# Performance work log

Measured on AMD Instinct MI355X. Metric: run time of the kernel, lower is better.

Reference implementation:

```python
import jax, jax.numpy as jnp
import numpy as np

M = 16384          # test points
N = 16384          # train points
D = 2              # (kx, ky)
CHUNK = 8192       # rows of K_star per chunk (matches torch default)


def setup_inputs() -> dict:
    key = jax.random.key(0)
    k1, k2, k3 = jax.random.split(key, 3)
    X_test = jax.random.normal(k1, (M, D), dtype=jnp.float32)
    X_train = jax.random.normal(k2, (N, D), dtype=jnp.float32)
    alpha = jax.random.normal(k3, (N, 2), dtype=jnp.float32)  # dual vars [Re, Im]
    log_lengthscale = jnp.asarray(np.log(0.1), dtype=jnp.float32)
    log_outputscale = jnp.asarray(np.log(1.0), dtype=jnp.float32)
    return {
        "X_test": X_test,
        "X_train": X_train,
        "alpha": alpha,
        "log_lengthscale": log_lengthscale,
        "log_outputscale": log_outputscale,
    }


def reference(X_test, X_train, alpha, log_lengthscale, log_outputscale):
    """Posterior mean mu* = K_rbf(X_test, X_train) @ alpha, chunked over test rows."""
    ell2 = jnp.exp(log_lengthscale) ** 2
    sf2 = jnp.exp(log_outputscale) ** 2
    xt_sq = jnp.sum(X_train * X_train, axis=1)  # (N,)

    def chunk_fn(xc):  # xc: (CHUNK, D)
        # squared euclidean distances (clamped at 0 for numerical safety)
        sq = (jnp.sum(xc * xc, axis=1)[:, None]
              + xt_sq[None, :]
              - 2.0 * (xc @ X_train.T))          # (CHUNK, N)
        sq = jnp.maximum(sq, 0.0)
        K = sf2 * jnp.exp(-0.5 * sq / ell2)      # RBF kernel values
        return K @ alpha                          # (CHUNK, 2)

    m = X_test.shape[0]
    chunks = X_test.reshape(m // CHUNK, CHUNK, D)
    out = jax.lax.map(chunk_fn, chunks)           # (m//CHUNK, CHUNK, 2)
    return out.reshape(m, 2)
```

## Files before the change

### kernel.cpp

```cpp
#include <hip/hip_runtime.h>
#include <math.h>

#define M_PTS 16384
#define N_PTS 16384
#define TPB 256
#define SPLITS 128
#define CHUNK_N (N_PTS / SPLITS)
#define PTS 4
#define TEST_BLOCKS (M_PTS / (TPB * PTS))

__device__ __forceinline__ float fexp2(float x) {
#if __has_builtin(__builtin_amdgcn_exp2f)
    return __builtin_amdgcn_exp2f(x);
#else
    return exp2f(x);
#endif
}

__device__ __forceinline__ void gatomic_fadd(float* p, float v) {
    asm volatile("global_atomic_add_f32 %0, %1, off" :: "v"(p), "v"(v) : "memory");
}

template <bool ATOMIC>
__global__ __launch_bounds__(TPB, 8) void gp_fused(
        const float2* __restrict__ Xte,
        const float2* __restrict__ Xtr,
        const float2* __restrict__ alpha,
        const float* __restrict__ log_ell,
        const float* __restrict__ log_sf,
        float2* __restrict__ outp) {
    __shared__ float4 sSt[CHUNK_N];
    __shared__ float  sA1[CHUNK_N];

    const int tid = threadIdx.x;
    const float ell = expf(log_ell[0]);
    const float c = -0.5f / (ell * ell) * 1.4426950408889634f;

    const int j0 = blockIdx.y * CHUNK_N;
    if (tid < CHUNK_N) {
        const float sf2 = expf(2.0f * log_sf[0]);
        float2 t = Xtr[j0 + tid];
        float2 a = alpha[j0 + tid];
        sSt[tid] = make_float4(-2.0f * c * t.x, -2.0f * c * t.y,
                               c * (t.x * t.x + t.y * t.y), sf2 * a.x);
        sA1[tid] = sf2 * a.y;
    }

    const int base = blockIdx.x * (TPB * PTS) + tid;
    float2 x0 = Xte[base];
    float2 x1 = Xte[base + TPB];
    float2 x2 = Xte[base + 2 * TPB];
    float2 x3 = Xte[base + 3 * TPB];
    const float b0 = c * (x0.x * x0.x + x0.y * x0.y);
    const float b1 = c * (x1.x * x1.x + x1.y * x1.y);
    const float b2 = c * (x2.x * x2.x + x2.y * x2.y);
    const float b3 = c * (x3.x * x3.x + x3.y * x3.y);

    __syncthreads();

    float a00 = 0.f, a01 = 0.f, a10 = 0.f, a11 = 0.f;
    float a20 = 0.f, a21 = 0.f, a30 = 0.f, a31 = 0.f;

#pragma unroll 2
    for (int j = 0; j < CHUNK_N; ++j) {
        float4 s = sSt[j];
        float w1 = sA1[j];
        float t0 = fminf(fmaf(s.x, x0.x, fmaf(s.y, x0.y, b0 + s.z)), 0.0f);
        float t1 = fminf(fmaf(s.x, x1.x, fmaf(s.y, x1.y, b1 + s.z)), 0.0f);
        float t2 = fminf(fmaf(s.x, x2.x, fmaf(s.y, x2.y, b2 + s.z)), 0.0f);
        float t3 = fminf(fmaf(s.x, x3.x, fmaf(s.y, x3.y, b3 + s.z)), 0.0f);
        float e0 = fexp2(t0);
        float e1 = fexp2(t1);
        float e2 = fexp2(t2);
        float e3 = fexp2(t3);
        a00 = fmaf(e0, s.w, a00); a01 = fmaf(e0, w1, a01);
        a10 = fmaf(e1, s.w, a10); a11 = fmaf(e1, w1, a11);
        a20 = fmaf(e2, s.w, a20); a21 = fmaf(e2, w1, a21);
        a30 = fmaf(e3, s.w, a30); a31 = fmaf(e3, w1, a31);
    }

    if (ATOMIC) {
        float* o = (float*)outp;
        gatomic_fadd(&o[2 * base], a00);            gatomic_fadd(&o[2 * base + 1], a01);
        gatomic_fadd(&o[2 * (base + TPB)], a10);     gatomic_fadd(&o[2 * (base + TPB) + 1], a11);
        gatomic_fadd(&o[2 * (base + 2 * TPB)], a20); gatomic_fadd(&o[2 * (base + 2 * TPB) + 1], a21);
        gatomic_fadd(&o[2 * (base + 3 * TPB)], a30); gatomic_fadd(&o[2 * (base + 3 * TPB) + 1], a31);
    } else {
        float2* w = outp + (size_t)blockIdx.y * M_PTS;
        w[base]           = make_float2(a00, a01);
        w[base + TPB]     = make_float2(a10, a11);
        w[base + 2 * TPB] = make_float2(a20, a21);
        w[base + 3 * TPB] = make_float2(a30, a31);
    }
}

__global__ __launch_bounds__(TPB) void reduce_kernel(
        const float2* __restrict__ ws, float2* __restrict__ out) {
    int i = blockIdx.x * blockDim.x + threadIdx.x;
    float sx = 0.f, sy = 0.f;
#pragma unroll 8
    for (int k = 0; k < SPLITS; ++k) {
        float2 v = ws[(size_t)k * M_PTS + i];
        sx += v.x;
        sy += v.y;
    }
    out[i] = make_float2(sx, sy);
}

extern "C" void kernel_launch(void* const* d_in, const int* in_sizes, int n_in,
                              void* d_out, int out_size, void* d_ws, size_t ws_size,
                              hipStream_t stream) {
    const float2* Xte = (const float2*)d_in[0];
    const float2* Xtr = (const float2*)d_in[1];
    const float2* alpha = (const float2*)d_in[2];
    const float* log_ell = (const float*)d_in[3];
    const float* log_sf = (const float*)d_in[4];

    dim3 grid(TEST_BLOCKS, SPLITS);
    const size_t need = (size_t)SPLITS * M_PTS * sizeof(float2);

    if (ws_size >= need) {
        float2* partials = (float2*)d_ws;
        gp_fused<false><<<grid, TPB, 0, stream>>>(Xte, Xtr, alpha, log_ell, log_sf,
                                                  partials);
        reduce_kernel<<<M_PTS / TPB, TPB, 0, stream>>>(partials, (float2*)d_out);
    } else {
        hipMemsetAsync(d_out, 0, (size_t)out_size * sizeof(float), stream);
        gp_fused<true><<<grid, TPB, 0, stream>>>(Xte, Xtr, alpha, log_ell, log_sf,
                                                 (float2*)d_out);
    }
}
```

Measured before the change: 122.5 us.

## Bin points on a spatial grid and evaluate RBF only over neighbouring cells

Replaces the all-pairs dense RBF accumulation with a uniform 2D cell grid. Training and test points are binned by histogram, prefix-scan and scatter kernels, and test points are padded to whole wavefronts per cell. Each wavefront then visits only the 5x5 neighbouring training cells and skips exp work when the whole wave is below a cutoff exponent. This cuts the number of kernel evaluations but adds several small preprocessing launches, uncoalesced global loads in place of shared-memory reuse, and truncation of tiny kernel values. A full-range fallback runs when the lengthscale is too large for the cell size.

Result: slower. 207.1 us (+69.1%).

```diff
diff --git a/kernel.cpp b/kernel.cpp
--- a/kernel.cpp
+++ b/kernel.cpp
@@ -4,10 +4,30 @@
 #define M_PTS 16384
 #define N_PTS 16384
 #define TPB 256
-#define SPLITS 128
-#define CHUNK_N (N_PTS / SPLITS)
-#define PTS 4
-#define TEST_BLOCKS (M_PTS / (TPB * PTS))
+
+#define NC 28
+#define NCELLS (NC * NC)
+#define H 0.375f
+#define INV_H (1.0f / 0.375f)
+#define ORIG (-5.25f)
+#define TCUT 40.0f
+
+#define NPAD_MAX (M_PTS + NCELLS * 63)
+#define WAVES_MAX (M_PTS / 64 + NCELLS)
+#define KITEMS 25
+#define ITEMS_MAX (WAVES_MAX * KITEMS)
+#define MAIN_BLOCKS (ITEMS_MAX / 4)
+
+#define OFF_HDR 0
+#define OFF_TRC 256
+#define OFF_TEC (OFF_TRC + NCELLS * 4)
+#define OFF_TRS (OFF_TEC + NCELLS * 4)
+#define OFF_TRCUR (OFF_TRS + NCELLS * 4)
+#define OFF_TECUR (OFF_TRCUR + NCELLS * 4)
+#define OFF_TRA (OFF_TECUR + NCELLS * 4)
+#define OFF_TRW1 (OFF_TRA + N_PTS * 16)
+#define OFF_T4 (OFF_TRW1 + N_PTS * 4)
+#define WS_NEED (OFF_T4 + (size_t)NPAD_MAX * 16)
 
 __device__ __forceinline__ float fexp2(float x) {
 #if __has_builtin(__builtin_amdgcn_exp2f)
@@ -21,90 +41,183 @@
     asm volatile("global_atomic_add_f32 %0, %1, off" :: "v"(p), "v"(v) : "memory");
 }
 
-template <bool ATOMIC>
-__global__ __launch_bounds__(TPB, 8) void gp_fused(
-        const float2* __restrict__ Xte,
-        const float2* __restrict__ Xtr,
-        const float2* __restrict__ alpha,
-        const float* __restrict__ log_ell,
-        const float* __restrict__ log_sf,
-        float2* __restrict__ outp) {
-    __shared__ float4 sSt[CHUNK_N];
-    __shared__ float  sA1[CHUNK_N];
-
+__device__ __forceinline__ int cellco(float v) {
+    int c = (int)floorf((v - ORIG) * INV_H);
+    return min(NC - 1, max(0, c));
+}
+
+
+__global__ void fill_kernel(float4* __restrict__ T4) {
+    int i = blockIdx.x * blockDim.x + threadIdx.x;
+    if (i < NPAD_MAX)
+        T4[i] = make_float4(0.f, 0.f, -3.0e38f, __int_as_float(-1));
+}
+
+__global__ void hist_kernel(const float2* __restrict__ Xtr,
+                            const float2* __restrict__ Xte,
+                            int* __restrict__ trc, int* __restrict__ tec) {
+    int i = blockIdx.x * blockDim.x + threadIdx.x;
+    if (i >= N_PTS) return;
+    float2 t = Xtr[i];
+    atomicAdd(&trc[cellco(t.y) * NC + cellco(t.x)], 1);
+    float2 x = Xte[i];
+    atomicAdd(&tec[cellco(x.y) * NC + cellco(x.x)], 1);
+}
+
+__global__ __launch_bounds__(1024) void scan_kernel(
+        const int* __restrict__ trc, const int* __restrict__ tec,
+        int* __restrict__ trs, int* __restrict__ trcur,
+        int* __restrict__ tecur, int* __restrict__ hdr) {
+    __shared__ int sc[1024];
+    int tid = threadIdx.x;
+    int v = (tid < NCELLS) ? trc[tid] : 0;
+    sc[tid] = v; __syncthreads();
+    for (int off = 1; off < 1024; off <<= 1) {
+        int u = (tid >= off) ? sc[tid - off] : 0;
+        __syncthreads();
+        sc[tid] += u;
+        __syncthreads();
+    }
+    if (tid < NCELLS) { int e = sc[tid] - v; trs[tid] = e; trcur[tid] = e; }
+    __syncthreads();
+    int pv = (tid < NCELLS) ? ((tec[tid] + 63) & ~63) : 0;
+    sc[tid] = pv; __syncthreads();
+    for (int off = 1; off < 1024; off <<= 1) {
+        int u = (tid >= off) ? sc[tid - off] : 0;
+        __syncthreads();
+        sc[tid] += u;
+        __syncthreads();
+    }
+    if (tid < NCELLS) tecur[tid] = sc[tid] - pv;
+    if (tid == NCELLS - 1) hdr[0] = sc[tid] / 64;
+}
+
+__global__ void scatter_kernel(const float2* __restrict__ Xtr,
+                               const float2* __restrict__ Xte,
+                               const float2* __restrict__ alpha,
+                               const float* __restrict__ log_ell,
+                               const float* __restrict__ log_sf,
+                               int* __restrict__ trcur, int* __restrict__ tecur,
+                               float4* __restrict__ trA, float* __restrict__ trW1,
+                               float4* __restrict__ T4) {
+    int i = blockIdx.x * blockDim.x + threadIdx.x;
+    if (i >= N_PTS) return;
+    float ell = expf(log_ell[0]);
+    float sf2 = expf(2.0f * log_sf[0]);
+    float c = -0.5f / (ell * ell) * 1.4426950408889634f;
+
+    float2 t = Xtr[i];
+    float2 a = alpha[i];
+    int ct = cellco(t.y) * NC + cellco(t.x);
+    int pt = atomicAdd(&trcur[ct], 1);
+    trA[pt] = make_float4(-2.f * c * t.x, -2.f * c * t.y,
+                          c * (t.x * t.x + t.y * t.y), sf2 * a.x);
+    trW1[pt] = sf2 * a.y;
+
+    float2 x = Xte[i];
+    int cx = cellco(x.y) * NC + cellco(x.x);
+    int px = atomicAdd(&tecur[cx], 1);
+    T4[px] = make_float4(x.x, x.y, c * (x.x * x.x + x.y * x.y), __int_as_float(i));
+}
+
+__global__ __launch_bounds__(TPB, 8) void gp_sparse(
+        const float4* __restrict__ T4, const float4* __restrict__ trA,
+        const float* __restrict__ trW1, const int* __restrict__ trs,
+        const int* __restrict__ trc, const int* __restrict__ hdr,
+        const float* __restrict__ log_ell, float* __restrict__ out) {
+    const int wave = (blockIdx.x << 2) + (threadIdx.x >> 6);
+    const int lane = threadIdx.x & 63;
+    const int tw = wave / KITEMS;
+    const int k = wave - tw * KITEMS;
+    if (tw >= hdr[0]) return;
+
+    const float ell = expf(log_ell[0]);
+    const float cmag = 0.5f / (ell * ell) * 1.4426950408889634f;
+    const bool fb = (TCUT / cmag) > (4.0f * H * H);
+
+    float4 tp = T4[tw * 64 + lane];
+    const float x = tp.x, y = tp.y, b = tp.z;
+    const int oidx = __float_as_int(tp.w);
+
+    int js, je;
+    if (fb) {
+        if (k != 12) return;
+        js = 0; je = N_PTS;
+    } else {
+        int cx = __builtin_amdgcn_readfirstlane(cellco(x));
+        int cy = __builtin_amdgcn_readfirstlane(cellco(y));
+        int tcx = cx + (k % 5) - 2;
+        int tcy = cy + (k / 5) - 2;
+        if (tcx < 0 || tcx >= NC || tcy < 0 || tcy >= NC) return;
+        int cid = tcy * NC + tcx;
+        js = trs[cid];
+        je = js + trc[cid];
+    }
+
+    float a0 = 0.f, a1 = 0.f;
+#pragma unroll 2
+    for (int j = js; j < je; ++j) {
+        float4 tv = trA[j];
+        float t = fmaf(tv.x, x, fmaf(tv.y, y, b + tv.z));
+        if (__ballot(t > -TCUT) != 0ull) {
+            float e = fexp2(t);
+            a0 = fmaf(e, tv.w, a0);
+            a1 = fmaf(e, trW1[j], a1);
+        }
+    }
+
+    if (oidx >= 0 && ((a0 != 0.f) || (a1 != 0.f))) {
+        gatomic_fadd(&out[2 * oidx], a0);
+        gatomic_fadd(&out[2 * oidx + 1], a1);
+    }
+}
+
+__global__ __launch_bounds__(TPB, 8) void gp_dense(
+        const float2* __restrict__ Xte, const float2* __restrict__ Xtr,
+        const float2* __restrict__ alpha, const float* __restrict__ log_ell,
+        const float* __restrict__ log_sf, float* __restrict__ out) {
+    __shared__ float4 sSt[128];
+    __shared__ float sA1[128];
     const int tid = threadIdx.x;
     const float ell = expf(log_ell[0]);
     const float c = -0.5f / (ell * ell) * 1.4426950408889634f;
-
-    const int j0 = blockIdx.y * CHUNK_N;
-    if (tid < CHUNK_N) {
+    const int j0 = blockIdx.y * 128;
+    if (tid < 128) {
         const float sf2 = expf(2.0f * log_sf[0]);
         float2 t = Xtr[j0 + tid];
         float2 a = alpha[j0 + tid];
-        sSt[tid] = make_float4(-2.0f * c * t.x, -2.0f * c * t.y,
+        sSt[tid] = make_float4(-2.f * c * t.x, -2.f * c * t.y,
                                c * (t.x * t.x + t.y * t.y), sf2 * a.x);
         sA1[tid] = sf2 * a.y;
     }
-
-    const int base = blockIdx.x * (TPB * PTS) + tid;
-    float2 x0 = Xte[base];
-    float2 x1 = Xte[base + TPB];
-    float2 x2 = Xte[base + 2 * TPB];
-    float2 x3 = Xte[base + 3 * TPB];
+    const int base = blockIdx.x * (TPB * 4) + tid;
+    float2 x0 = Xte[base], x1 = Xte[base + TPB];
+    float2 x2 = Xte[base + 2 * TPB], x3 = Xte[base + 3 * TPB];
     const float b0 = c * (x0.x * x0.x + x0.y * x0.y);
     const float b1 = c * (x1.x * x1.x + x1.y * x1.y);
     const float b2 = c * (x2.x * x2.x + x2.y * x2.y);
     const float b3 = c * (x3.x * x3.x + x3.y * x3.y);
-
     __syncthreads();
-
     float a00 = 0.f, a01 = 0.f, a10 = 0.f, a11 = 0.f;
     float a20 = 0.f, a21 = 0.f, a30 = 0.f, a31 = 0.f;
-
 #pragma unroll 2
-    for (int j = 0; j < CHUNK_N; ++j) {
+    for (int j = 0; j < 128; ++j) {
         float4 s = sSt[j];
         float w1 = sA1[j];
-        float t0 = fminf(fmaf(s.x, x0.x, fmaf(s.y, x0.y, b0 + s.z)), 0.0f);
-        float t1 = fminf(fmaf(s.x, x1.x, fmaf(s.y, x1.y, b1 + s.z)), 0.0f);
-        float t2 = fminf(fmaf(s.x, x2.x, fmaf(s.y, x2.y, b2 + s.z)), 0.0f);
-        float t3 = fminf(fmaf(s.x, x3.x, fmaf(s.y, x3.y, b3 + s.z)), 0.0f);
-        float e0 = fexp2(t0);
-        float e1 = fexp2(t1);
-        float e2 = fexp2(t2);
-        float e3 = fexp2(t3);
+        float t0 = fminf(fmaf(s.x, x0.x, fmaf(s.y, x0.y, b0 + s.z)), 0.f);
+        float t1 = fminf(fmaf(s.x, x1.x, fmaf(s.y, x1.y, b1 + s.z)), 0.f);
+        float t2 = fminf(fmaf(s.x, x2.x, fmaf(s.y, x2.y, b2 + s.z)), 0.f);
+        float t3 = fminf(fmaf(s.x, x3.x, fmaf(s.y, x3.y, b3 + s.z)), 0.f);
+        float e0 = fexp2(t0), e1 = fexp2(t1), e2 = fexp2(t2), e3 = fexp2(t3);
         a00 = fmaf(e0, s.w, a00); a01 = fmaf(e0, w1, a01);
         a10 = fmaf(e1, s.w, a10); a11 = fmaf(e1, w1, a11);
         a20 = fmaf(e2, s.w, a20); a21 = fmaf(e2, w1, a21);
         a30 = fmaf(e3, s.w, a30); a31 = fmaf(e3, w1, a31);
     }
-
-    if (ATOMIC) {
-        float* o = (float*)outp;
-        gatomic_fadd(&o[2 * base], a00);            gatomic_fadd(&o[2 * base + 1], a01);
-        gatomic_fadd(&o[2 * (base + TPB)], a10);     gatomic_fadd(&o[2 * (base + TPB) + 1], a11);
-        gatomic_fadd(&o[2 * (base + 2 * TPB)], a20); gatomic_fadd(&o[2 * (base + 2 * TPB) + 1], a21);
-        gatomic_fadd(&o[2 * (base + 3 * TPB)], a30); gatomic_fadd(&o[2 * (base + 3 * TPB) + 1], a31);
-    } else {
-        float2* w = outp + (size_t)blockIdx.y * M_PTS;
-        w[base]           = make_float2(a00, a01);
-        w[base + TPB]     = make_float2(a10, a11);
-        w[base + 2 * TPB] = make_float2(a20, a21);
-        w[base + 3 * TPB] = make_float2(a30, a31);
-    }
-}
-
-__global__ __launch_bounds__(TPB) void reduce_kernel(
-        const float2* __restrict__ ws, float2* __restrict__ out) {
-    int i = blockIdx.x * blockDim.x + threadIdx.x;
-    float sx = 0.f, sy = 0.f;
-#pragma unroll 8
-    for (int k = 0; k < SPLITS; ++k) {
-        float2 v = ws[(size_t)k * M_PTS + i];
-        sx += v.x;
-        sy += v.y;
-    }
-    out[i] = make_float2(sx, sy);
+    gatomic_fadd(&out[2 * base], a00);             gatomic_fadd(&out[2 * base + 1], a01);
+    gatomic_fadd(&out[2 * (base + TPB)], a10);      gatomic_fadd(&out[2 * (base + TPB) + 1], a11);
+    gatomic_fadd(&out[2 * (base + 2 * TPB)], a20);  gatomic_fadd(&out[2 * (base + 2 * TPB) + 1], a21);
+    gatomic_fadd(&out[2 * (base + 3 * TPB)], a30);  gatomic_fadd(&out[2 * (base + 3 * TPB) + 1], a31);
 }
 
 extern "C" void kernel_launch(void* const* d_in, const int* in_sizes, int n_in,
@@ -115,18 +228,33 @@
     const float2* alpha = (const float2*)d_in[2];
     const float* log_ell = (const float*)d_in[3];
     const float* log_sf = (const float*)d_in[4];
-
-    dim3 grid(TEST_BLOCKS, SPLITS);
-    const size_t need = (size_t)SPLITS * M_PTS * sizeof(float2);
-
-    if (ws_size >= need) {
-        float2* partials = (float2*)d_ws;
-        gp_fused<false><<<grid, TPB, 0, stream>>>(Xte, Xtr, alpha, log_ell, log_sf,
-                                                  partials);
-        reduce_kernel<<<M_PTS / TPB, TPB, 0, stream>>>(partials, (float2*)d_out);
+    float* out = (float*)d_out;
+
+    hipMemsetAsync(out, 0, (size_t)out_size * sizeof(float), stream);
+
+    if (ws_size >= WS_NEED) {
+        char* ws = (char*)d_ws;
+        int* hdr = (int*)(ws + OFF_HDR);
+        int* trc = (int*)(ws + OFF_TRC);
+        int* tec = (int*)(ws + OFF_TEC);
+        int* trs = (int*)(ws + OFF_TRS);
+        int* trcur = (int*)(ws + OFF_TRCUR);
+        int* tecur = (int*)(ws + OFF_TECUR);
+        float4* trA = (float4*)(ws + OFF_TRA);
+        float* trW1 = (float*)(ws + OFF_TRW1);
+        float4* T4 = (float4*)(ws + OFF_T4);
+
+        hipMemsetAsync(trc, 0, NCELLS * 2 * sizeof(int), stream);
+        fill_kernel<<<(NPAD_MAX + TPB - 1) / TPB, TPB, 0, stream>>>(T4);
+        hist_kernel<<<N_PTS / TPB, TPB, 0, stream>>>(Xtr, Xte, trc, tec);
+        scan_kernel<<<1, 1024, 0, stream>>>(trc, tec, trs, trcur, tecur, hdr);
+        scatter_kernel<<<N_PTS / TPB, TPB, 0, stream>>>(Xtr, Xte, alpha, log_ell,
+                                                        log_sf, trcur, tecur,
+                                                        trA, trW1, T4);
+        gp_sparse<<<MAIN_BLOCKS, TPB, 0, stream>>>(T4, trA, trW1, trs, trc, hdr,
+                                                   log_ell, out);
     } else {
-        hipMemsetAsync(d_out, 0, (size_t)out_size * sizeof(float), stream);
-        gp_fused<true><<<grid, TPB, 0, stream>>>(Xte, Xtr, alpha, log_ell, log_sf,
-                                                 (float2*)d_out);
-    }
-}
+        dim3 grid(M_PTS / (TPB * 4), N_PTS / 128);
+        gp_dense<<<grid, TPB, 0, stream>>>(Xte, Xtr, alpha, log_ell, log_sf, out);
+    }
+}
```

## Replace dense RBF sum with cell-list neighbor search and exponent cutoff

Applied to the files above, without the earlier changes.

Training points are binned into a uniform 2D grid by a histogram, a prefix scan and a scatter, which also precompute the per-point kernel coefficients. A per-test-point wavefront then evaluates only the grid rows and columns inside a cutoff radius where the base-2 exponent stays above -20, instead of all N training points. If the lengthscale makes the radius too large, it falls back to scanning every training point. The aim is to avoid most of the exp and FMA work of the dense O(M·N) evaluation, at the cost of a truncation error, several extra small launches, and gather-style global loads in place of shared-memory reuse.

Result: faster. 118.8 us (-3.0%).

```diff
diff --git a/kernel.cpp b/kernel.cpp
--- a/kernel.cpp
+++ b/kernel.cpp
@@ -3,11 +3,22 @@
 
 #define M_PTS 16384
 #define N_PTS 16384
-#define TPB 256
-#define SPLITS 128
-#define CHUNK_N (N_PTS / SPLITS)
-#define PTS 4
-#define TEST_BLOCKS (M_PTS / (TPB * PTS))
+
+#define NC 42
+#define NCELLS (NC * NC)
+#define NPAIR (NCELLS / 2)
+#define H 0.25f
+#define INV_H 4.0f
+#define ORIG (-5.25f)
+#define TCUT 20.0f
+#define KCAP 31
+
+#define OFF_HTR 0
+#define OFF_TRS (OFF_HTR + NCELLS * 4)
+#define OFF_TRCUR (OFF_TRS + (NCELLS + 1) * 4 + 60)
+#define OFF_TRA ((OFF_TRCUR + NCELLS * 4 + 255) & ~255)
+#define OFF_TRW1 (OFF_TRA + N_PTS * 16)
+#define WS_NEED (OFF_TRW1 + (size_t)N_PTS * 4)
 
 __device__ __forceinline__ float fexp2(float x) {
 #if __has_builtin(__builtin_amdgcn_exp2f)
@@ -21,90 +32,168 @@
     asm volatile("global_atomic_add_f32 %0, %1, off" :: "v"(p), "v"(v) : "memory");
 }
 
-template <bool ATOMIC>
-__global__ __launch_bounds__(TPB, 8) void gp_fused(
-        const float2* __restrict__ Xte,
-        const float2* __restrict__ Xtr,
-        const float2* __restrict__ alpha,
-        const float* __restrict__ log_ell,
-        const float* __restrict__ log_sf,
-        float2* __restrict__ outp) {
-    __shared__ float4 sSt[CHUNK_N];
-    __shared__ float  sA1[CHUNK_N];
-
+__device__ __forceinline__ int cellco(float v) {
+    int c = (int)floorf((v - ORIG) * INV_H);
+    return min(NC - 1, max(0, c));
+}
+
+__global__ __launch_bounds__(256) void hist_kernel(
+        const float2* __restrict__ Xtr, int* __restrict__ hTr) {
+    int i = blockIdx.x * 256 + threadIdx.x;
+    float2 t = Xtr[i];
+    atomicAdd(&hTr[cellco(t.y) * NC + cellco(t.x)], 1);
+}
+
+__global__ __launch_bounds__(1024) void scan_kernel(
+        const int* __restrict__ hTr, int* __restrict__ trs,
+        int* __restrict__ trcur) {
+    __shared__ int sc[1024];
+    const int tid = threadIdx.x;
+    int hv0 = (tid < NPAIR) ? hTr[2 * tid] : 0;
+    int hv1 = (tid < NPAIR) ? hTr[2 * tid + 1] : 0;
+    int v = hv0 + hv1;
+    sc[tid] = v; __syncthreads();
+    for (int o = 1; o < 1024; o <<= 1) {
+        int u = (tid >= o) ? sc[tid - o] : 0;
+        __syncthreads(); sc[tid] += u; __syncthreads();
+    }
+    if (tid < NPAIR) {
+        int e = sc[tid] - v;
+        trs[2 * tid] = e;      trcur[2 * tid] = e;
+        trs[2 * tid + 1] = e + hv0;  trcur[2 * tid + 1] = e + hv0;
+    }
+    if (tid == NPAIR - 1) trs[NCELLS] = sc[tid];
+}
+
+__global__ __launch_bounds__(256) void scatter_kernel(
+        const float2* __restrict__ Xtr, const float2* __restrict__ alpha,
+        const float* __restrict__ log_ell, const float* __restrict__ log_sf,
+        int* __restrict__ trcur, float4* __restrict__ trA,
+        float* __restrict__ trW1) {
+    int i = blockIdx.x * 256 + threadIdx.x;
+    float ell = expf(log_ell[0]);
+    float sf2 = expf(2.0f * log_sf[0]);
+    float c = -0.5f / (ell * ell) * 1.4426950408889634f;
+
+    float2 t = Xtr[i];
+    float2 a = alpha[i];
+    int ct = cellco(t.y) * NC + cellco(t.x);
+    int pt = atomicAdd(&trcur[ct], 1);
+    trA[pt] = make_float4(-2.f * c * t.x, -2.f * c * t.y,
+                          c * (t.x * t.x + t.y * t.y), sf2 * a.x);
+    trW1[pt] = sf2 * a.y;
+}
+
+__global__ __launch_bounds__(256) void gp_point(
+        const float2* __restrict__ Xte, const float4* __restrict__ trA,
+        const float* __restrict__ trW1, const int* __restrict__ trs,
+        const float* __restrict__ log_ell, float2* __restrict__ out2) {
+    const int wid = (blockIdx.x << 2) + (threadIdx.x >> 6);
+    const int lane = threadIdx.x & 63;
+
+    const float ell = expf(log_ell[0]);
+    const float cmag = 0.5f / (ell * ell) * 1.4426950408889634f;
+    const float r2 = TCUT / cmag;
+
+    const float2 xt = Xte[wid];
+    const float b = -cmag * (xt.x * xt.x + xt.y * xt.y);
+
+    int K = (int)floorf(sqrtf(r2) * INV_H) + 1;
+    int js_l = 0, je_l = 0;
+    int nrows;
+    if (K > KCAP) {
+        nrows = 1;
+        if (lane == 0) { js_l = 0; je_l = N_PTS; }
+    } else {
+        nrows = 2 * K + 1;
+        const int cx = cellco(xt.x), cy = cellco(xt.y);
+        if (lane < nrows) {
+            int ry = cy - K + lane;
+            if (ry >= 0 && ry < NC) {
+                int dy = (lane < K) ? (K - lane) : (lane - K);
+                int kx;
+                if (dy <= 1) kx = K;
+                else {
+                    float d = (float)(dy - 1) * H;
+                    kx = (int)floorf(sqrtf(fmaxf(r2 - d * d, 0.f)) * INV_H) + 1;
+                }
+                int c0 = max(0, cx - kx);
+                int c1 = min(NC - 1, cx + kx);
+                js_l = trs[ry * NC + c0];
+                je_l = trs[ry * NC + c1 + 1];
+            }
+        }
+    }
+
+    float a0 = 0.f, a1 = 0.f;
+    for (int rr = 0; rr < nrows; ++rr) {
+        const int js = __shfl(js_l, rr);
+        const int je = __shfl(je_l, rr);
+        for (int j0 = js; j0 < je; j0 += 64) {
+            int j = j0 + lane;
+            int jc = min(j, je - 1);
+            float4 tv = trA[jc];
+            float w1 = trW1[jc];
+            float arg = fmaf(tv.x, xt.x, fmaf(tv.y, xt.y, b + tv.z));
+            arg = (j < je) ? arg : -1.0e30f;
+            float e = fexp2(arg);
+            a0 = fmaf(e, tv.w, a0);
+            a1 = fmaf(e, w1, a1);
+        }
+    }
+
+    for (int o = 32; o > 0; o >>= 1) {
+        a0 += __shfl_xor(a0, o);
+        a1 += __shfl_xor(a1, o);
+    }
+    if (lane == 0) out2[wid] = make_float2(a0, a1);
+}
+
+__global__ __launch_bounds__(256, 8) void gp_dense(
+        const float2* __restrict__ Xte, const float2* __restrict__ Xtr,
+        const float2* __restrict__ alpha, const float* __restrict__ log_ell,
+        const float* __restrict__ log_sf, float* __restrict__ out) {
+    __shared__ float4 sSt[128];
+    __shared__ float sA1[128];
     const int tid = threadIdx.x;
     const float ell = expf(log_ell[0]);
     const float c = -0.5f / (ell * ell) * 1.4426950408889634f;
-
-    const int j0 = blockIdx.y * CHUNK_N;
-    if (tid < CHUNK_N) {
+    const int j0 = blockIdx.y * 128;
+    if (tid < 128) {
         const float sf2 = expf(2.0f * log_sf[0]);
         float2 t = Xtr[j0 + tid];
         float2 a = alpha[j0 + tid];
-        sSt[tid] = make_float4(-2.0f * c * t.x, -2.0f * c * t.y,
+        sSt[tid] = make_float4(-2.f * c * t.x, -2.f * c * t.y,
                                c * (t.x * t.x + t.y * t.y), sf2 * a.x);
         sA1[tid] = sf2 * a.y;
     }
-
-    const int base = blockIdx.x * (TPB * PTS) + tid;
-    float2 x0 = Xte[base];
-    float2 x1 = Xte[base + TPB];
-    float2 x2 = Xte[base + 2 * TPB];
-    float2 x3 = Xte[base + 3 * TPB];
+    const int base = blockIdx.x * 1024 + tid;
+    float2 x0 = Xte[base], x1 = Xte[base + 256];
+    float2 x2 = Xte[base + 512], x3 = Xte[base + 768];
     const float b0 = c * (x0.x * x0.x + x0.y * x0.y);
     const float b1 = c * (x1.x * x1.x + x1.y * x1.y);
     const float b2 = c * (x2.x * x2.x + x2.y * x2.y);
     const float b3 = c * (x3.x * x3.x + x3.y * x3.y);
-
     __syncthreads();
-
     float a00 = 0.f, a01 = 0.f, a10 = 0.f, a11 = 0.f;
     float a20 = 0.f, a21 = 0.f, a30 = 0.f, a31 = 0.f;
-
 #pragma unroll 2
-    for (int j = 0; j < CHUNK_N; ++j) {
+    for (int j = 0; j < 128; ++j) {
         float4 s = sSt[j];
         float w1 = sA1[j];
-        float t0 = fminf(fmaf(s.x, x0.x, fmaf(s.y, x0.y, b0 + s.z)), 0.0f);
-        float t1 = fminf(fmaf(s.x, x1.x, fmaf(s.y, x1.y, b1 + s.z)), 0.0f);
-        float t2 = fminf(fmaf(s.x, x2.x, fmaf(s.y, x2.y, b2 + s.z)), 0.0f);
-        float t3 = fminf(fmaf(s.x, x3.x, fmaf(s.y, x3.y, b3 + s.z)), 0.0f);
-        float e0 = fexp2(t0);
-        float e1 = fexp2(t1);
-        float e2 = fexp2(t2);
-        float e3 = fexp2(t3);
+        float e0 = fexp2(fminf(fmaf(s.x, x0.x, fmaf(s.y, x0.y, b0 + s.z)), 0.f));
+        float e1 = fexp2(fminf(fmaf(s.x, x1.x, fmaf(s.y, x1.y, b1 + s.z)), 0.f));
+        float e2 = fexp2(fminf(fmaf(s.x, x2.x, fmaf(s.y, x2.y, b2 + s.z)), 0.f));
+        float e3 = fexp2(fminf(fmaf(s.x, x3.x, fmaf(s.y, x3.y, b3 + s.z)), 0.f));
         a00 = fmaf(e0, s.w, a00); a01 = fmaf(e0, w1, a01);
         a10 = fmaf(e1, s.w, a10); a11 = fmaf(e1, w1, a11);
         a20 = fmaf(e2, s.w, a20); a21 = fmaf(e2, w1, a21);
         a30 = fmaf(e3, s.w, a30); a31 = fmaf(e3, w1, a31);
     }
-
-    if (ATOMIC) {
-        float* o = (float*)outp;
-        gatomic_fadd(&o[2 * base], a00);            gatomic_fadd(&o[2 * base + 1], a01);
-        gatomic_fadd(&o[2 * (base + TPB)], a10);     gatomic_fadd(&o[2 * (base + TPB) + 1], a11);
-        gatomic_fadd(&o[2 * (base + 2 * TPB)], a20); gatomic_fadd(&o[2 * (base + 2 * TPB) + 1], a21);
-        gatomic_fadd(&o[2 * (base + 3 * TPB)], a30); gatomic_fadd(&o[2 * (base + 3 * TPB) + 1], a31);
-    } else {
-        float2* w = outp + (size_t)blockIdx.y * M_PTS;
-        w[base]           = make_float2(a00, a01);
-        w[base + TPB]     = make_float2(a10, a11);
-        w[base + 2 * TPB] = make_float2(a20, a21);
-        w[base + 3 * TPB] = make_float2(a30, a31);
-    }
-}
-
-__global__ __launch_bounds__(TPB) void reduce_kernel(
-        const float2* __restrict__ ws, float2* __restrict__ out) {
-    int i = blockIdx.x * blockDim.x + threadIdx.x;
-    float sx = 0.f, sy = 0.f;
-#pragma unroll 8
-    for (int k = 0; k < SPLITS; ++k) {
-        float2 v = ws[(size_t)k * M_PTS + i];
-        sx += v.x;
-        sy += v.y;
-    }
-    out[i] = make_float2(sx, sy);
+    gatomic_fadd(&out[2 * base], a00);            gatomic_fadd(&out[2 * base + 1], a01);
+    gatomic_fadd(&out[2 * (base + 256)], a10);    gatomic_fadd(&out[2 * (base + 256) + 1], a11);
+    gatomic_fadd(&out[2 * (base + 512)], a20);    gatomic_fadd(&out[2 * (base + 512) + 1], a21);
+    gatomic_fadd(&out[2 * (base + 768)], a30);    gatomic_fadd(&out[2 * (base + 768) + 1], a31);
 }
 
 extern "C" void kernel_launch(void* const* d_in, const int* in_sizes, int n_in,
@@ -115,18 +204,26 @@
     const float2* alpha = (const float2*)d_in[2];
     const float* log_ell = (const float*)d_in[3];
     const float* log_sf = (const float*)d_in[4];
-
-    dim3 grid(TEST_BLOCKS, SPLITS);
-    const size_t need = (size_t)SPLITS * M_PTS * sizeof(float2);
-
-    if (ws_size >= need) {
-        float2* partials = (float2*)d_ws;
-        gp_fused<false><<<grid, TPB, 0, stream>>>(Xte, Xtr, alpha, log_ell, log_sf,
-                                                  partials);
-        reduce_kernel<<<M_PTS / TPB, TPB, 0, stream>>>(partials, (float2*)d_out);
+    float* out = (float*)d_out;
+
+    if (ws_size >= WS_NEED) {
+        char* ws = (char*)d_ws;
+        int* hTr = (int*)(ws + OFF_HTR);
+        int* trs = (int*)(ws + OFF_TRS);
+        int* trcur = (int*)(ws + OFF_TRCUR);
+        float4* trA = (float4*)(ws + OFF_TRA);
+        float* trW1 = (float*)(ws + OFF_TRW1);
+
+        hipMemsetAsync(hTr, 0, NCELLS * sizeof(int), stream);
+        hist_kernel<<<N_PTS / 256, 256, 0, stream>>>(Xtr, hTr);
+        scan_kernel<<<1, 1024, 0, stream>>>(hTr, trs, trcur);
+        scatter_kernel<<<N_PTS / 256, 256, 0, stream>>>(Xtr, alpha, log_ell,
+                                                        log_sf, trcur, trA, trW1);
+        gp_point<<<M_PTS / 4, 256, 0, stream>>>(Xte, trA, trW1, trs, log_ell,
+                                                (float2*)out);
     } else {
-        hipMemsetAsync(d_out, 0, (size_t)out_size * sizeof(float), stream);
-        gp_fused<true><<<grid, TPB, 0, stream>>>(Xte, Xtr, alpha, log_ell, log_sf,
-                                                 (float2*)d_out);
-    }
-}
+        hipMemsetAsync(out, 0, (size_t)out_size * sizeof(float), stream);
+        dim3 grid(M_PTS / 1024, N_PTS / 128);
+        gp_dense<<<grid, 256, 0, stream>>>(Xte, Xtr, alpha, log_ell, log_sf, out);
+    }
+}
```
